# Kernel tuning notes

Hardware: AMD Instinct MI355X
Metric: run time of the kernel (lower is better)

The kernel has to match this reference:

```python
import jax, jax.numpy as jnp
import numpy as np

E = 128       # embed_dim
H = 128       # hidden_dim
NLABEL = 5
VOCAB = 50000
DEPTH = 18    # levels 0..17, complete binary tree
BRANCH = 2
N_NODES = 2 ** DEPTH - 1  # level-order layout: level l occupies [2^l-1, 2^(l+1)-1)


def setup_inputs() -> dict:
    key = jax.random.key(0)
    ks = jax.random.split(key, 24)

    def w(k, shape):
        return jax.random.normal(k, shape, dtype=jnp.float32) * 0.05

    inp = {
        "embeds": w(ks[0], (VOCAB, E)),
        "node_words": jax.random.randint(ks[1], (N_NODES,), 0, VOCAB),
        "node_labels": jax.random.randint(ks[2], (N_NODES,), 0, NLABEL),
        "depth": DEPTH,
        "branching": BRANCH,
    }
    # 8 gate linears: *x maps E->H, *h maps H->H (torch nn.Linear: y = x @ W.T + b)
    for j, nm in enumerate(["ix", "ih", "fx", "fh", "ox", "oh", "ux", "uh"]):
        in_dim = E if nm.endswith("x") else H
        inp["W" + nm] = w(ks[3 + 2 * j], (H, in_dim))
        inp["b" + nm] = w(ks[4 + 2 * j], (H,))
    inp["Wout"] = w(ks[20], (NLABEL, H))
    inp["bout"] = w(ks[21], (NLABEL,))
    return inp


def _lin(x, W, b):
    return x @ W.T + b


def _tree_lstm(embeds, node_words, node_labels, depth, branching,
               Wix, bix, Wih, bih, Wfx, bfx, Wfh, bfh,
               Wox, box, Woh, boh, Wux, bux, Wuh, buh, Wout, bout):
    b = branching
    hid = Wix.shape[0]
    loss = jnp.zeros((), dtype=embeds.dtype)
    child_c = child_h = None
    logp = None
    # bottom-up over levels (leaves first); level l has b^l nodes at offset (b^l-1)/(b-1)
    for l in range(depth - 1, -1, -1):
        n = b ** l
        off = (b ** l - 1) // (b - 1)
        x = embeds[node_words[off:off + n]]            # [n, E]
        if child_h is None:                            # leaves: zero child states
            h_sum = jnp.zeros((n, hid), dtype=embeds.dtype)
            c_agg = jnp.zeros((n, hid), dtype=embeds.dtype)
        else:
            ch = child_h.reshape(n, b, hid)            # children of each level-l node
            cc = child_c.reshape(n, b, hid)
            h_sum = ch.sum(axis=1)                     # child-sum
            f = jax.nn.sigmoid(_lin(x, Wfx, bfx)[:, None, :] + _lin(ch, Wfh, bfh))
            c_agg = (f * cc).sum(axis=1)               # sum_k f_k * c_k
        i = jax.nn.sigmoid(_lin(x, Wix, bix) + _lin(h_sum, Wih, bih))
        o = jax.nn.sigmoid(_lin(x, Wox, box) + _lin(h_sum, Woh, boh))
        u = jnp.tanh(_lin(x, Wux, bux) + _lin(h_sum, Wuh, buh))
        c = i * u + c_agg
        h = o * jnp.tanh(c)
        logp = jax.nn.log_softmax(_lin(h, Wout, bout), axis=-1)   # [n, NLABEL]
        lab = node_labels[off:off + n]
        loss = loss - logp[jnp.arange(n), lab].sum()              # NLL summed over nodes
        child_c, child_h = c, h
    return logp, loss  # logp from level 0 = root log-probs [1, NLABEL]


def reference(embeds, node_words, node_labels, depth, branching,
              Wix, bix, Wih, bih, Wfx, bfx, Wfh, bfh,
              Wox, box, Woh, boh, Wux, bux, Wuh, buh, Wout, bout):
    return _tree_lstm(embeds, node_words, node_labels, depth, branching,
                      Wix, bix, Wih, bih, Wfx, bfx, Wfh, bfh,
                      Wox, box, Woh, boh, Wux, bux, Wuh, buh, Wout, bout)
```

## Files before the change

kernel.cpp:

```cpp
#include <hip/hip_runtime.h>
#include <math.h>

#define DEPTH 18
#define NINT ((1 << (DEPTH - 1)) - 1)
#define LEAF_OFF ((1 << (DEPTH - 2)) - 1)
#define NVOCAB 50000
#define SAW 520
#define KTS 9
#define NEMB (NVOCAB * 128 / 4 / 256)

typedef unsigned short bf16raw;
typedef __bf16 bf16x8 __attribute__((ext_vector_type(8)));
typedef float f32x4 __attribute__((ext_vector_type(4)));
typedef short short8 __attribute__((ext_vector_type(8)));

__device__ __forceinline__ float sigm(float x) { return 1.0f / (1.0f + __expf(-x)); }
__device__ __forceinline__ float fast_tanh(float x) {
    float t = __expf(2.0f * x);
    return 1.0f - 2.0f / (t + 1.0f);
}

__device__ __forceinline__ float bf2f(bf16raw u) {
    union { unsigned int i; float f; } v;
    v.i = ((unsigned int)u) << 16;
    return v.f;
}
__device__ __forceinline__ bf16raw f2bf(float f) {
    union { float f; unsigned int i; } v;
    v.f = f;
    unsigned int r = v.i + 0x7FFFu + ((v.i >> 16) & 1u);
    return (bf16raw)(r >> 16);
}

#define SB() __builtin_amdgcn_sched_barrier(0)

__global__ __launch_bounds__(256) void k_prep_all(
    const float* __restrict__ embeds,
    const float* __restrict__ Wix, const float* __restrict__ bix,
    const float* __restrict__ Wih, const float* __restrict__ bih,
    const float* __restrict__ Wfx, const float* __restrict__ bfx,
    const float* __restrict__ Wfh, const float* __restrict__ bfh,
    const float* __restrict__ Wox, const float* __restrict__ box_,
    const float* __restrict__ Woh, const float* __restrict__ boh,
    const float* __restrict__ Wux, const float* __restrict__ bux,
    const float* __restrict__ Wuh, const float* __restrict__ buh,
    const float* __restrict__ Wout,
    bf16raw* __restrict__ embeds_bf,
    bf16raw* __restrict__ Bfrag, bf16raw* __restrict__ WoutFrag,
    float* __restrict__ bias_cat, float* __restrict__ partials)
{
    const int bid = blockIdx.x;
    const int t = threadIdx.x;
    if (bid < NEMB) {
        const int i = bid * 256 + t;
        float4 v = ((const float4*)embeds)[i];
        ushort4 o;
        o.x = f2bf(v.x); o.y = f2bf(v.y); o.z = f2bf(v.z); o.w = f2bf(v.w);
        ((ushort4*)embeds_bf)[i] = o;
        return;
    }
    if (bid == NEMB + 528) {
#pragma unroll
        for (int s = 0; s < 4; ++s) partials[t + 256 * s] = 0.f;
        return;
    }
    const int j = bid - NEMB;
    if (j >= 512) {
        const int col = j - 512;
        for (int k = t; k < 128; k += 256) {
            float v = (col < 5) ? Wout[col * 128 + k] : 0.f;
            WoutFrag[((k >> 5) * 64 + ((k >> 3) & 3) * 16 + col) * 8 + (k & 7)] = f2bf(v);
        }
        return;
    }
    const int gate = j >> 7, jj = j & 127;
    const float *Wx, *Wh, *bx, *bh;
    switch (gate) {
        case 0: Wx = Wix; Wh = Wih; bx = bix;  bh = bih; break;
        case 1: Wx = Wux; Wh = Wuh; bx = bux;  bh = buh; break;
        case 2: Wx = Wox; Wh = Woh; bx = box_; bh = boh; break;
        default: Wx = Wfx; Wh = Wfh; bx = bfx; bh = bfh; break;
    }
    const int coltile = (j >> 4) & 7, lr = j & 15;
    for (int k = t; k < 256; k += 256) {
        float v = (k < 128) ? Wx[jj * 128 + k] : Wh[jj * 128 + (k - 128)];
        const int idx = (((gate * 8 + coltile) * KTS + (k >> 5)) * 64
                         + ((k >> 3) & 3) * 16 + lr) * 8 + (k & 7);
        Bfrag[idx] = f2bf(v);
    }
    if (t == 0) bias_cat[j] = bx[jj] + bh[jj];
}

template<int CB>
__device__ __forceinline__ void lp_burst(const bf16raw* __restrict__ bfbase, int wcol,
                                         bf16x8 (&bb)[16])
{
#pragma unroll
    for (int kt = 0; kt < 4; ++kt)
#pragma unroll
        for (int j = 0; j < 4; ++j)
            bb[kt * 4 + j] = *(const bf16x8*)(bfbase +
                    (long)(((CB * 8 + (wcol >> 4) + j) * KTS + kt) * 512));
}

__device__ __forceinline__ void lp_mfma_all(const bf16raw* __restrict__ sA, int wrow,
                                            int lrow, int lquad,
                                            bf16x8 (&bb)[16], f32x4 (&acc)[2][4])
{
#pragma unroll
    for (int kt = 0; kt < 4; ++kt) {
        bf16x8 af[2];
#pragma unroll
        for (int i = 0; i < 2; ++i)
            af[i] = *(const bf16x8*)&sA[(wrow + i * 16 + lrow) * 136 + kt * 32 + lquad * 8];
#pragma unroll
        for (int i = 0; i < 2; ++i)
#pragma unroll
            for (int j = 0; j < 4; ++j)
                acc[i][j] = __builtin_amdgcn_mfma_f32_16x16x32_bf16(af[i], bb[kt * 4 + j], acc[i][j], 0, 0, 0);
    }
}

template<int CB>
__device__ __forceinline__ void lp_rungemm(const bf16raw* __restrict__ sA,
                                           const bf16raw* __restrict__ bfbase,
                                           int wrow, int wcol, int lrow, int lquad,
                                           f32x4 (&acc)[2][4])
{
#pragma unroll
    for (int i = 0; i < 2; i++)
#pragma unroll
        for (int j = 0; j < 4; j++) acc[i][j] = (f32x4){0.f, 0.f, 0.f, 0.f};
    bf16x8 bb[16];
    lp_burst<CB>(bfbase, wcol, bb);
    SB();
    lp_mfma_all(sA, wrow, lrow, lquad, bb, acc);
}

template<int G, int H>
__device__ __forceinline__ void load8(const bf16raw* __restrict__ bfbase, int w,
                                      bf16x8 (&bb)[8])
{
#pragma unroll
    for (int kt2 = 0; kt2 < 4; ++kt2)
#pragma unroll
        for (int jj = 0; jj < 2; ++jj)
            bb[kt2 * 2 + jj] = *(const bf16x8*)(bfbase +
                    (long)(((G * 8 + w * 2 + jj) * KTS + H * 4 + kt2) * 512));
}

template<int AB>
__device__ __forceinline__ void mfma4k(const bf16raw* __restrict__ sA, int lrow, int lquad,
                                       bf16x8 (&bb)[8], f32x4 (&acc)[2][2])
{
#pragma unroll
    for (int kt2 = 0; kt2 < 4; ++kt2) {
        bf16x8 af[2];
#pragma unroll
        for (int i = 0; i < 2; ++i)
            af[i] = *(const bf16x8*)&sA[(i * 16 + lrow) * SAW + (AB + kt2) * 32 + lquad * 8];
#pragma unroll
        for (int jj = 0; jj < 2; ++jj)
#pragma unroll
            for (int i = 0; i < 2; ++i)
                acc[i][jj] = __builtin_amdgcn_mfma_f32_16x16x32_bf16(af[i], bb[kt2 * 2 + jj], acc[i][jj], 0, 0, 0);
    }
}

__global__ __launch_bounds__(256, 3) void k_leafpre(
    const bf16raw* __restrict__ embeds_bf,
    const bf16raw* __restrict__ Bfrag, const float* __restrict__ bias_cat,
    const bf16raw* __restrict__ WoutFrag, const float* __restrict__ bout,
    bf16raw* __restrict__ hc_leaf, float* __restrict__ lossv6, int nvtot)
{
    const int vbase = blockIdx.x * 64;
    int nv = nvtot - vbase;
    if (nv > 64) nv = 64;
    if (nv <= 0) return;

    __shared__ __align__(16) bf16raw sA[64 * 136];
    __shared__ __align__(16) bf16raw sT[64 * 136];
    __shared__ float sLg[64 * 5];

    const int t = threadIdx.x;

    {
        const int row = t >> 2;
        const int co = (t & 3) * 32;
        const int arow = (row < nv) ? row : 0;
        const bf16raw* ax = embeds_bf + (long)(vbase + arow) * 128;
        *(short8*)&sA[row * 136 + co]      = *(const short8*)(ax + co);
        *(short8*)&sA[row * 136 + co + 8]  = *(const short8*)(ax + co + 8);
        *(short8*)&sA[row * 136 + co + 16] = *(const short8*)(ax + co + 16);
        *(short8*)&sA[row * 136 + co + 24] = *(const short8*)(ax + co + 24);
    }

    const int lane = t & 63;
    const int w = t >> 6;
    const int wrow = (w & 1) * 32;
    const int wcol = (w >> 1) * 64;
    const int lrow = lane & 15;
    const int lquad = lane >> 4;

    __syncthreads();

    const bf16raw* bfbase = Bfrag + (long)lane * 8;

    float tval[2][4][4];
    f32x4 acc[2][4];

    lp_rungemm<0>(sA, bfbase, wrow, wcol, lrow, lquad, acc);
#pragma unroll
    for (int i = 0; i < 2; i++)
#pragma unroll
        for (int jj = 0; jj < 4; jj++) {
            const float b = bias_cat[wcol + jj * 16 + lrow];
#pragma unroll
            for (int r = 0; r < 4; r++) tval[i][jj][r] = sigm(acc[i][jj][r] + b);
        }
    lp_rungemm<1>(sA, bfbase, wrow, wcol, lrow, lquad, acc);
#pragma unroll
    for (int i = 0; i < 2; i++)
#pragma unroll
        for (int jj = 0; jj < 4; jj++) {
            const float b = bias_cat[128 + wcol + jj * 16 + lrow];
#pragma unroll
            for (int r = 0; r < 4; r++) tval[i][jj][r] *= fast_tanh(acc[i][jj][r] + b);
        }
#pragma unroll
    for (int i = 0; i < 2; i++)
#pragma unroll
        for (int jj = 0; jj < 4; jj++)
#pragma unroll
            for (int r = 0; r < 4; r++) {
                const int m = wrow + i * 16 + lquad * 4 + r;
                const int j = wcol + jj * 16 + lrow;
                sT[m * 136 + j] = f2bf(tval[i][jj][r]);
            }
#pragma unroll
    for (int i = 0; i < 2; i++)
#pragma unroll
        for (int jj = 0; jj < 4; jj++)
#pragma unroll
            for (int r = 0; r < 4; r++) tval[i][jj][r] = fast_tanh(tval[i][jj][r]);
    __syncthreads();
#pragma unroll
    for (int s = 0; s < 4; ++s) {
        int ci = t + 256 * s;
        int row = ci >> 4, c8 = (ci & 15) * 8;
        if (row < nv)
            *(short8*)(hc_leaf + (long)(vbase + row) * 256 + 128 + c8) = *(const short8*)&sT[row * 136 + c8];
    }
    lp_rungemm<2>(sA, bfbase, wrow, wcol, lrow, lquad, acc);
    __syncthreads();
#pragma unroll
    for (int i = 0; i < 2; i++)
#pragma unroll
        for (int jj = 0; jj < 4; jj++) {
            const float b = bias_cat[256 + wcol + jj * 16 + lrow];
#pragma unroll
            for (int r = 0; r < 4; r++) {
                const int m = wrow + i * 16 + lquad * 4 + r;
                const int j = wcol + jj * 16 + lrow;
                sT[m * 136 + j] = f2bf(sigm(acc[i][jj][r] + b) * tval[i][jj][r]);
            }
        }
    __syncthreads();
#pragma unroll
    for (int s = 0; s < 4; ++s) {
        int ci = t + 256 * s;
        int row = ci >> 4, c8 = (ci & 15) * 8;
        if (row < nv)
            *(short8*)(hc_leaf + (long)(vbase + row) * 256 + c8) = *(const short8*)&sT[row * 136 + c8];
    }
    {
        f32x4 lacc = (f32x4){0.f, 0.f, 0.f, 0.f};
#pragma unroll
        for (int kt = 0; kt < 4; ++kt) {
            bf16x8 bfr = *(const bf16x8*)(WoutFrag + (long)((kt * 64 + lane) * 8));
            bf16x8 af = *(const bf16x8*)&sT[(w * 16 + lrow) * 136 + kt * 32 + lquad * 8];
            lacc = __builtin_amdgcn_mfma_f32_16x16x32_bf16(af, bfr, lacc, 0, 0, 0);
        }
        if (lrow < 5) {
            const float bl = bout[lrow];
#pragma unroll
            for (int r = 0; r < 4; ++r)
                sLg[(w * 16 + lquad * 4 + r) * 5 + lrow] = lacc[r] + bl;
        }
    }
    __syncthreads();
    if (t < 64 && t < nv) {
        float lg[5], mx = -1e30f;
#pragma unroll
        for (int l = 0; l < 5; l++) {
            lg[l] = sLg[t * 5 + l];
            mx = fmaxf(mx, lg[l]);
        }
        float se = 0.f;
#pragma unroll
        for (int l = 0; l < 5; l++) se += __expf(lg[l] - mx);
        float lse = __logf(se) + mx;
        float* dst = lossv6 + (long)(vbase + t) * 6;
#pragma unroll
        for (int l = 0; l < 5; l++) dst[l] = lg[l];
        dst[5] = lse;
    }
}

__global__ __launch_bounds__(256, 3) void k_level32(
    const bf16raw* __restrict__ embeds_bf, const int* __restrict__ words,
    const int* __restrict__ labels,
    bf16raw* __restrict__ h_all, bf16raw* __restrict__ c_all,
    const bf16raw* __restrict__ hc_leaf, const float* __restrict__ lossv6,
    const bf16raw* __restrict__ Bfrag, const bf16raw* __restrict__ WoutFrag,
    const float* __restrict__ bias_cat, const float* __restrict__ bout,
    float* __restrict__ partials, float* __restrict__ out,
    int off, int nm, int leafkids, int isroot)
{
    __shared__ __align__(16) bf16raw sA[32 * SAW];
    __shared__ __align__(16) bf16raw sCT[64 * 136];
    __shared__ float sLg[168];

    const int t = threadIdx.x;
    const int m0 = blockIdx.x * 32;

    {
        const int row = t >> 3;
        const int co = (t & 7) * 8;
        int mm = m0 + row; if (mm >= nm) mm = nm - 1;
        const long g = (long)off + mm;
        const bf16raw* px = embeds_bf + (long)words[g] * 128;
        const bf16raw *p1, *p2;
        if (leafkids) {
            p1 = hc_leaf + (long)words[2 * g + 1] * 256;
            p2 = hc_leaf + (long)words[2 * g + 2] * 256;
        } else {
            p1 = h_all + (2 * g + 1) * 128;
            p2 = h_all + (2 * g + 2) * 128;
        }
        short8 vx0 = *(const short8*)(px + co);
        short8 vx1 = *(const short8*)(px + 64 + co);
        short8 h10 = *(const short8*)(p1 + co);
        short8 h11 = *(const short8*)(p1 + 64 + co);
        short8 h20 = *(const short8*)(p2 + co);
        short8 h21 = *(const short8*)(p2 + 64 + co);
        short8 hs0, hs1;
#pragma unroll
        for (int e = 0; e < 8; ++e) {
            hs0[e] = (short)f2bf(bf2f((bf16raw)(unsigned short)h10[e]) +
                                 bf2f((bf16raw)(unsigned short)h20[e]));
            hs1[e] = (short)f2bf(bf2f((bf16raw)(unsigned short)h11[e]) +
                                 bf2f((bf16raw)(unsigned short)h21[e]));
        }
        *(short8*)&sA[row * SAW + co]        = vx0;
        *(short8*)&sA[row * SAW + 64 + co]   = vx1;
        *(short8*)&sA[row * SAW + 128 + co]  = hs0;
        *(short8*)&sA[row * SAW + 192 + co]  = hs1;
        *(short8*)&sA[row * SAW + 256 + co]  = h10;
        *(short8*)&sA[row * SAW + 320 + co]  = h11;
        *(short8*)&sA[row * SAW + 384 + co]  = h20;
        *(short8*)&sA[row * SAW + 448 + co]  = h21;
    }
    {
        const int slot = t >> 2;
        const int cc8 = (t & 3) * 8;
        int mm = m0 + (slot >> 1); if (mm >= nm) mm = nm - 1;
        const long g = (long)off + mm;
        const long cg = 2 * g + 1 + (slot & 1);
        const bf16raw* pc = leafkids ? (hc_leaf + (long)words[cg] * 256 + 128)
                                     : (c_all + cg * 128);
#pragma unroll
        for (int s = 0; s < 4; ++s)
            *(short8*)&sCT[slot * 136 + s * 32 + cc8] = *(const short8*)(pc + s * 32 + cc8);
    }

    const int lane = t & 63;
    const int w = t >> 6;
    const int lrow = lane & 15;
    const int lquad = lane >> 4;

    float bias[4][2];
#pragma unroll
    for (int g = 0; g < 4; ++g)
#pragma unroll
        for (int jj = 0; jj < 2; ++jj)
            bias[g][jj] = bias_cat[g * 128 + w * 32 + jj * 16 + lrow];

    __syncthreads();

    const bf16raw* bfbase = Bfrag + (long)lane * 8;

    f32x4 acc[2][2];
    f32x4 fx[2][2];
    float si[2][2][4];
    float cc[2][2][4];
    float hh[2][2][4];
    bf16x8 bbA[8], bbB[8];

#define ZACC() { _Pragma("unroll") for (int i_ = 0; i_ < 2; ++i_) \
                 _Pragma("unroll") for (int j_ = 0; j_ < 2; ++j_) \
                     acc[i_][j_] = (f32x4){0.f, 0.f, 0.f, 0.f}; }

    load8<0, 0>(bfbase, w, bbA);
    load8<0, 1>(bfbase, w, bbB);
    SB();
    ZACC();
    mfma4k<0>(sA, lrow, lquad, bbA, acc); SB();
    load8<1, 0>(bfbase, w, bbA); SB();
    mfma4k<4>(sA, lrow, lquad, bbB, acc); SB();
    load8<1, 1>(bfbase, w, bbB); SB();
#pragma unroll
    for (int i = 0; i < 2; ++i)
#pragma unroll
        for (int jj = 0; jj < 2; ++jj)
#pragma unroll
            for (int r = 0; r < 4; ++r)
                si[i][jj][r] = sigm(acc[i][jj][r] + bias[0][jj]);
    ZACC();
    mfma4k<0>(sA, lrow, lquad, bbA, acc); SB();
    load8<3, 0>(bfbase, w, bbA); SB();
    mfma4k<4>(sA, lrow, lquad, bbB, acc); SB();
    load8<3, 1>(bfbase, w, bbB); SB();
#pragma unroll
    for (int i = 0; i < 2; ++i)
#pragma unroll
        for (int jj = 0; jj < 2; ++jj)
#pragma unroll
            for (int r = 0; r < 4; ++r)
                cc[i][jj][r] = si[i][jj][r] * fast_tanh(acc[i][jj][r] + bias[1][jj]);
    ZACC();
    mfma4k<0>(sA, lrow, lquad, bbA, acc);
    SB();
#pragma unroll
    for (int i = 0; i < 2; ++i)
#pragma unroll
        for (int jj = 0; jj < 2; ++jj) fx[i][jj] = acc[i][jj];
    mfma4k<8>(sA, lrow, lquad, bbB, acc);
    SB();
    load8<2, 0>(bfbase, w, bbA);
    SB();
#pragma unroll
    for (int i = 0; i < 2; ++i)
#pragma unroll
        for (int jj = 0; jj < 2; ++jj) {
            const int j = w * 32 + jj * 16 + lrow;
#pragma unroll
            for (int r = 0; r < 4; ++r) {
                const int m = i * 16 + lquad * 4 + r;
                cc[i][jj][r] += sigm(acc[i][jj][r] + bias[3][jj]) * bf2f(sCT[(2 * m) * 136 + j]);
            }
        }
#pragma unroll
    for (int i = 0; i < 2; ++i)
#pragma unroll
        for (int jj = 0; jj < 2; ++jj) acc[i][jj] = fx[i][jj];
    mfma4k<12>(sA, lrow, lquad, bbB, acc);
    SB();
    load8<2, 1>(bfbase, w, bbB);
    SB();
#pragma unroll
    for (int i = 0; i < 2; ++i)
#pragma unroll
        for (int jj = 0; jj < 2; ++jj) {
            const int j = w * 32 + jj * 16 + lrow;
#pragma unroll
            for (int r = 0; r < 4; ++r) {
                const int m = i * 16 + lquad * 4 + r;
                cc[i][jj][r] += sigm(acc[i][jj][r] + bias[3][jj]) * bf2f(sCT[(2 * m + 1) * 136 + j]);
            }
        }
    ZACC();
    mfma4k<0>(sA, lrow, lquad, bbA, acc);
    mfma4k<4>(sA, lrow, lquad, bbB, acc);
    SB();
#pragma unroll
    for (int i = 0; i < 2; ++i)
#pragma unroll
        for (int jj = 0; jj < 2; ++jj)
#pragma unroll
            for (int r = 0; r < 4; ++r)
                hh[i][jj][r] = sigm(acc[i][jj][r] + bias[2][jj]) * fast_tanh(cc[i][jj][r]);
#undef ZACC

    __syncthreads();

#pragma unroll
    for (int i = 0; i < 2; ++i)
#pragma unroll
        for (int jj = 0; jj < 2; ++jj) {
            const int j = w * 32 + jj * 16 + lrow;
#pragma unroll
            for (int r = 0; r < 4; ++r) {
                const int m = i * 16 + lquad * 4 + r;
                sCT[m * 136 + j] = f2bf(cc[i][jj][r]);
                sCT[(32 + m) * 136 + j] = f2bf(hh[i][jj][r]);
            }
        }
    __syncthreads();

#pragma unroll
    for (int q = 0; q < 4; ++q) {
        int ci = t + 256 * q;
        int row = ci >> 4;
        int c8 = (ci & 15) * 8;
        int m = row & 31;
        if (m0 + m < nm) {
            bf16raw* dst = (row < 32) ? c_all : h_all;
            *(short8*)(dst + ((long)off + m0 + m) * 128 + c8) = *(const short8*)&sCT[row * 136 + c8];
        }
    }

    if (w == 0) {
        f32x4 lacc[2];
        lacc[0] = (f32x4){0.f, 0.f, 0.f, 0.f};
        lacc[1] = (f32x4){0.f, 0.f, 0.f, 0.f};
#pragma unroll
        for (int kt = 0; kt < 4; ++kt) {
            bf16x8 bfr = *(const bf16x8*)(WoutFrag + (long)((kt * 64 + lane) * 8));
#pragma unroll
            for (int i = 0; i < 2; ++i) {
                bf16x8 af = *(const bf16x8*)&sCT[(32 + i * 16 + lrow) * 136 + kt * 32 + lquad * 8];
                lacc[i] = __builtin_amdgcn_mfma_f32_16x16x32_bf16(af, bfr, lacc[i], 0, 0, 0);
            }
        }
        if (lrow < 5) {
            const float bl = bout[lrow];
#pragma unroll
            for (int i = 0; i < 2; ++i)
#pragma unroll
                for (int r = 0; r < 4; ++r)
                    sLg[(i * 16 + lquad * 4 + r) * 5 + lrow] = lacc[i][r] + bl;
        }
    }
    __syncthreads();

    if (t < 32 && m0 + t < nm) {
        const long g = (long)off + m0 + t;
        float lgv[5], mx = -1e30f;
#pragma unroll
        for (int l = 0; l < 5; ++l) {
            lgv[l] = sLg[t * 5 + l];
            mx = fmaxf(mx, lgv[l]);
        }
        float se = 0.f;
#pragma unroll
        for (int l = 0; l < 5; ++l) se += __expf(lgv[l] - mx);
        float lse = __logf(se) + mx;
        float lossNode = lse - lgv[labels[g]];
        if (leafkids) {
            const float* lv1 = lossv6 + (long)words[2 * g + 1] * 6;
            const float* lv2 = lossv6 + (long)words[2 * g + 2] * 6;
            lossNode += (lv1[5] - lv1[labels[2 * g + 1]])
                      + (lv2[5] - lv2[labels[2 * g + 2]]);
        }
        if (isroot) {
            sLg[164] = lossNode;
#pragma unroll
            for (int l = 0; l < 5; ++l) out[l] = lgv[l] - lse;
        } else {
            atomicAdd(&partials[(int)(g & 1023)], lossNode);
        }
    }

    if (isroot) {
        __syncthreads();
        float s = 0.f;
        for (int i2 = t; i2 < 1024; i2 += 256) s += partials[i2];
#pragma unroll
        for (int d = 32; d > 0; d >>= 1) s += __shfl_down(s, d);
        if ((t & 63) == 0) sLg[160 + (t >> 6)] = s;
        __syncthreads();
        if (t == 0)
            out[5] = sLg[160] + sLg[161] + sLg[162] + sLg[163] + sLg[164];
    }
}

extern "C" void kernel_launch(void* const* d_in, const int* in_sizes, int n_in,
                              void* d_out, int out_size, void* d_ws, size_t ws_size,
                              hipStream_t stream)
{
    const float* embeds = (const float*)d_in[0];
    const int* words = (const int*)d_in[1];
    const int* labels = (const int*)d_in[2];
    const float* Wix = (const float*)d_in[5],  *bix  = (const float*)d_in[6];
    const float* Wih = (const float*)d_in[7],  *bih  = (const float*)d_in[8];
    const float* Wfx = (const float*)d_in[9],  *bfx  = (const float*)d_in[10];
    const float* Wfh = (const float*)d_in[11], *bfh  = (const float*)d_in[12];
    const float* Wox = (const float*)d_in[13], *box_ = (const float*)d_in[14];
    const float* Woh = (const float*)d_in[15], *boh  = (const float*)d_in[16];
    const float* Wux = (const float*)d_in[17], *bux  = (const float*)d_in[18];
    const float* Wuh = (const float*)d_in[19], *buh  = (const float*)d_in[20];
    const float* Wout = (const float*)d_in[21], *bout = (const float*)d_in[22];
    float* out = (float*)d_out;

    char* ws = (char*)d_ws;
    const size_t treeElems = (size_t)NINT * 128;
    bf16raw* h_all = (bf16raw*)ws;
    bf16raw* c_all = h_all + treeElems;
    bf16raw* embeds_bf = c_all + treeElems;
    bf16raw* Bfrag = embeds_bf + (size_t)NVOCAB * 128;
    bf16raw* WoutFrag = Bfrag + 4 * 8 * KTS * 512;
    bf16raw* hc_leaf = WoutFrag + 4 * 64 * 8;
    float* lossv6 = (float*)(hc_leaf + (size_t)NVOCAB * 256);
    float* bias_cat = lossv6 + (size_t)NVOCAB * 6;
    float* partials = bias_cat + 512;

    k_prep_all<<<NEMB + 528 + 1, 256, 0, stream>>>(
        embeds, Wix, bix, Wih, bih, Wfx, bfx, Wfh, bfh,
        Wox, box_, Woh, boh, Wux, bux, Wuh, buh, Wout,
        embeds_bf, Bfrag, WoutFrag, bias_cat, partials);

    k_leafpre<<<(NVOCAB + 63) / 64, 256, 0, stream>>>(
        embeds_bf, Bfrag, bias_cat, WoutFrag, bout, hc_leaf, lossv6, NVOCAB);

    for (int l = DEPTH - 2; l >= 0; --l) {
        const int n = 1 << l;
        k_level32<<<dim3((n + 31) / 32), 256, 0, stream>>>(
            embeds_bf, words, labels, h_all, c_all, hc_leaf, lossv6,
            Bfrag, WoutFrag, bias_cat, bout, partials, out,
            n - 1, n, (l == DEPTH - 2) ? 1 : 0, (l == 0) ? 1 : 0);
    }
}
```

Before: 366.5 us.

## Fuse two tree levels per launch with in-block parent computation

```diff
diff --git a/kernel.cpp b/kernel.cpp
--- a/kernel.cpp
+++ b/kernel.cpp
@@ -3,7 +3,6 @@
 
 #define DEPTH 18
 #define NINT ((1 << (DEPTH - 1)) - 1)
-#define LEAF_OFF ((1 << (DEPTH - 2)) - 1)
 #define NVOCAB 50000
 #define SAW 520
 #define KTS 9
@@ -167,6 +166,19 @@
     }
 }
 
+template<int AB>
+__device__ __forceinline__ void mfma4k1(const bf16raw* __restrict__ sA, int lrow, int lquad,
+                                        bf16x8 (&bb)[8], f32x4 (&acc)[2])
+{
+#pragma unroll
+    for (int kt2 = 0; kt2 < 4; ++kt2) {
+        bf16x8 af = *(const bf16x8*)&sA[lrow * SAW + (AB + kt2) * 32 + lquad * 8];
+#pragma unroll
+        for (int jj = 0; jj < 2; ++jj)
+            acc[jj] = __builtin_amdgcn_mfma_f32_16x16x32_bf16(af, bb[kt2 * 2 + jj], acc[jj], 0, 0, 0);
+    }
+}
+
 __global__ __launch_bounds__(256, 3) void k_leafpre(
     const bf16raw* __restrict__ embeds_bf,
     const bf16raw* __restrict__ Bfrag, const float* __restrict__ bias_cat,
@@ -304,6 +316,402 @@
 #pragma unroll
         for (int l = 0; l < 5; l++) dst[l] = lg[l];
         dst[5] = lse;
+    }
+}
+
+__global__ __launch_bounds__(256, 3) void k_pair(
+    const bf16raw* __restrict__ embeds_bf, const int* __restrict__ words,
+    const int* __restrict__ labels,
+    bf16raw* __restrict__ h_all, bf16raw* __restrict__ c_all,
+    const bf16raw* __restrict__ hc_leaf, const float* __restrict__ lossv6,
+    const bf16raw* __restrict__ Bfrag, const bf16raw* __restrict__ WoutFrag,
+    const float* __restrict__ bias_cat, const float* __restrict__ bout,
+    float* __restrict__ partials,
+    int offP, int nP, int leafkids)
+{
+    __shared__ __align__(16) bf16raw sA[32 * SAW];
+    __shared__ __align__(16) bf16raw sCT[64 * 136];
+    __shared__ float sLg[160];
+
+    const int t = threadIdx.x;
+    const int offC = 2 * offP + 1;
+    const int nmC = 2 * nP;
+    const int m0C = blockIdx.x * 32;
+    const int m0P = blockIdx.x * 16;
+
+    const int lane = t & 63;
+    const int w = t >> 6;
+    const int lrow = lane & 15;
+    const int lquad = lane >> 4;
+    const bf16raw* bfbase = Bfrag + (long)lane * 8;
+
+    float bias[4][2];
+#pragma unroll
+    for (int g = 0; g < 4; ++g)
+#pragma unroll
+        for (int jj = 0; jj < 2; ++jj)
+            bias[g][jj] = bias_cat[g * 128 + w * 32 + jj * 16 + lrow];
+
+    {
+        const int row = t >> 3;
+        const int co = (t & 7) * 8;
+        int mm = m0C + row; if (mm >= nmC) mm = nmC - 1;
+        const long g = (long)offC + mm;
+        const bf16raw* px = embeds_bf + (long)words[g] * 128;
+        const bf16raw *p1, *p2;
+        if (leafkids) {
+            p1 = hc_leaf + (long)words[2 * g + 1] * 256;
+            p2 = hc_leaf + (long)words[2 * g + 2] * 256;
+        } else {
+            p1 = h_all + (2 * g + 1) * 128;
+            p2 = h_all + (2 * g + 2) * 128;
+        }
+        short8 vx0 = *(const short8*)(px + co);
+        short8 vx1 = *(const short8*)(px + 64 + co);
+        short8 h10 = *(const short8*)(p1 + co);
+        short8 h11 = *(const short8*)(p1 + 64 + co);
+        short8 h20 = *(const short8*)(p2 + co);
+        short8 h21 = *(const short8*)(p2 + 64 + co);
+        short8 hs0, hs1;
+#pragma unroll
+        for (int e = 0; e < 8; ++e) {
+            hs0[e] = (short)f2bf(bf2f((bf16raw)(unsigned short)h10[e]) +
+                                 bf2f((bf16raw)(unsigned short)h20[e]));
+            hs1[e] = (short)f2bf(bf2f((bf16raw)(unsigned short)h11[e]) +
+                                 bf2f((bf16raw)(unsigned short)h21[e]));
+        }
+        *(short8*)&sA[row * SAW + co]        = vx0;
+        *(short8*)&sA[row * SAW + 64 + co]   = vx1;
+        *(short8*)&sA[row * SAW + 128 + co]  = hs0;
+        *(short8*)&sA[row * SAW + 192 + co]  = hs1;
+        *(short8*)&sA[row * SAW + 256 + co]  = h10;
+        *(short8*)&sA[row * SAW + 320 + co]  = h11;
+        *(short8*)&sA[row * SAW + 384 + co]  = h20;
+        *(short8*)&sA[row * SAW + 448 + co]  = h21;
+    }
+    {
+        const int slot = t >> 2;
+        const int cc8 = (t & 3) * 8;
+        int mm = m0C + (slot >> 1); if (mm >= nmC) mm = nmC - 1;
+        const long g = (long)offC + mm;
+        const long cg = 2 * g + 1 + (slot & 1);
+        const bf16raw* pc = leafkids ? (hc_leaf + (long)words[cg] * 256 + 128)
+                                     : (c_all + cg * 128);
+#pragma unroll
+        for (int s = 0; s < 4; ++s)
+            *(short8*)&sCT[slot * 136 + s * 32 + cc8] = *(const short8*)(pc + s * 32 + cc8);
+    }
+    __syncthreads();
+
+    {
+        f32x4 acc[2][2];
+        f32x4 fx[2][2];
+        float si[2][2][4];
+        float cc[2][2][4];
+        float hh[2][2][4];
+        bf16x8 bbA[8], bbB[8];
+
+#define ZACC() { _Pragma("unroll") for (int i_ = 0; i_ < 2; ++i_) \
+                 _Pragma("unroll") for (int j_ = 0; j_ < 2; ++j_) \
+                     acc[i_][j_] = (f32x4){0.f, 0.f, 0.f, 0.f}; }
+
+        load8<0, 0>(bfbase, w, bbA);
+        load8<0, 1>(bfbase, w, bbB);
+        SB();
+        ZACC();
+        mfma4k<0>(sA, lrow, lquad, bbA, acc); SB();
+        load8<1, 0>(bfbase, w, bbA); SB();
+        mfma4k<4>(sA, lrow, lquad, bbB, acc); SB();
+        load8<1, 1>(bfbase, w, bbB); SB();
+#pragma unroll
+        for (int i = 0; i < 2; ++i)
+#pragma unroll
+            for (int jj = 0; jj < 2; ++jj)
+#pragma unroll
+                for (int r = 0; r < 4; ++r)
+                    si[i][jj][r] = sigm(acc[i][jj][r] + bias[0][jj]);
+        ZACC();
+        mfma4k<0>(sA, lrow, lquad, bbA, acc); SB();
+        load8<3, 0>(bfbase, w, bbA); SB();
+        mfma4k<4>(sA, lrow, lquad, bbB, acc); SB();
+        load8<3, 1>(bfbase, w, bbB); SB();
+#pragma unroll
+        for (int i = 0; i < 2; ++i)
+#pragma unroll
+            for (int jj = 0; jj < 2; ++jj)
+#pragma unroll
+                for (int r = 0; r < 4; ++r)
+                    cc[i][jj][r] = si[i][jj][r] * fast_tanh(acc[i][jj][r] + bias[1][jj]);
+        ZACC();
+        mfma4k<0>(sA, lrow, lquad, bbA, acc);
+        SB();
+#pragma unroll
+        for (int i = 0; i < 2; ++i)
+#pragma unroll
+            for (int jj = 0; jj < 2; ++jj) fx[i][jj] = acc[i][jj];
+        mfma4k<8>(sA, lrow, lquad, bbB, acc);
+        SB();
+        load8<2, 0>(bfbase, w, bbA);
+        SB();
+#pragma unroll
+        for (int i = 0; i < 2; ++i)
+#pragma unroll
+            for (int jj = 0; jj < 2; ++jj) {
+                const int j = w * 32 + jj * 16 + lrow;
+#pragma unroll
+                for (int r = 0; r < 4; ++r) {
+                    const int m = i * 16 + lquad * 4 + r;
+                    cc[i][jj][r] += sigm(acc[i][jj][r] + bias[3][jj]) * bf2f(sCT[(2 * m) * 136 + j]);
+                }
+            }
+#pragma unroll
+        for (int i = 0; i < 2; ++i)
+#pragma unroll
+            for (int jj = 0; jj < 2; ++jj) acc[i][jj] = fx[i][jj];
+        mfma4k<12>(sA, lrow, lquad, bbB, acc);
+        SB();
+        load8<2, 1>(bfbase, w, bbB);
+        SB();
+#pragma unroll
+        for (int i = 0; i < 2; ++i)
+#pragma unroll
+            for (int jj = 0; jj < 2; ++jj) {
+                const int j = w * 32 + jj * 16 + lrow;
+#pragma unroll
+                for (int r = 0; r < 4; ++r) {
+                    const int m = i * 16 + lquad * 4 + r;
+                    cc[i][jj][r] += sigm(acc[i][jj][r] + bias[3][jj]) * bf2f(sCT[(2 * m + 1) * 136 + j]);
+                }
+            }
+        ZACC();
+        mfma4k<0>(sA, lrow, lquad, bbA, acc);
+        mfma4k<4>(sA, lrow, lquad, bbB, acc);
+        SB();
+#pragma unroll
+        for (int i = 0; i < 2; ++i)
+#pragma unroll
+            for (int jj = 0; jj < 2; ++jj)
+#pragma unroll
+                for (int r = 0; r < 4; ++r)
+                    hh[i][jj][r] = sigm(acc[i][jj][r] + bias[2][jj]) * fast_tanh(cc[i][jj][r]);
+#undef ZACC
+
+        __syncthreads();
+
+#pragma unroll
+        for (int i = 0; i < 2; ++i)
+#pragma unroll
+            for (int jj = 0; jj < 2; ++jj) {
+                const int j = w * 32 + jj * 16 + lrow;
+#pragma unroll
+                for (int r = 0; r < 4; ++r) {
+                    const int m = i * 16 + lquad * 4 + r;
+                    sCT[m * 136 + j] = f2bf(cc[i][jj][r]);
+                    sCT[(32 + m) * 136 + j] = f2bf(hh[i][jj][r]);
+                }
+            }
+    }
+    __syncthreads();
+
+    if (w == 0) {
+        f32x4 lacc[2];
+        lacc[0] = (f32x4){0.f, 0.f, 0.f, 0.f};
+        lacc[1] = (f32x4){0.f, 0.f, 0.f, 0.f};
+#pragma unroll
+        for (int kt = 0; kt < 4; ++kt) {
+            bf16x8 bfr = *(const bf16x8*)(WoutFrag + (long)((kt * 64 + lane) * 8));
+#pragma unroll
+            for (int i = 0; i < 2; ++i) {
+                bf16x8 af = *(const bf16x8*)&sCT[(32 + i * 16 + lrow) * 136 + kt * 32 + lquad * 8];
+                lacc[i] = __builtin_amdgcn_mfma_f32_16x16x32_bf16(af, bfr, lacc[i], 0, 0, 0);
+            }
+        }
+        if (lrow < 5) {
+            const float bl = bout[lrow];
+#pragma unroll
+            for (int i = 0; i < 2; ++i)
+#pragma unroll
+                for (int r = 0; r < 4; ++r)
+                    sLg[(i * 16 + lquad * 4 + r) * 5 + lrow] = lacc[i][r] + bl;
+        }
+    }
+    __syncthreads();
+
+    if (t < 32 && m0C + t < nmC) {
+        const long g = (long)offC + m0C + t;
+        float lgv[5], mx = -1e30f;
+#pragma unroll
+        for (int l = 0; l < 5; ++l) {
+            lgv[l] = sLg[t * 5 + l];
+            mx = fmaxf(mx, lgv[l]);
+        }
+        float se = 0.f;
+#pragma unroll
+        for (int l = 0; l < 5; ++l) se += __expf(lgv[l] - mx);
+        float lse = __logf(se) + mx;
+        float lossNode = lse - lgv[labels[g]];
+        if (leafkids) {
+            const float* lv1 = lossv6 + (long)words[2 * g + 1] * 6;
+            const float* lv2 = lossv6 + (long)words[2 * g + 2] * 6;
+            lossNode += (lv1[5] - lv1[labels[2 * g + 1]])
+                      + (lv2[5] - lv2[labels[2 * g + 2]]);
+        }
+        atomicAdd(&partials[(int)(g & 1023)], lossNode);
+    }
+    {
+        const int rowP = t >> 4;
+        const int co = (t & 15) * 8;
+        int pp = m0P + rowP; if (pp >= nP) pp = nP - 1;
+        const long gP = (long)offP + pp;
+        const int dp = pp - m0P;
+        const bf16raw* px = embeds_bf + (long)words[gP] * 128;
+        short8 vx = *(const short8*)(px + co);
+        short8 h1 = *(short8*)&sCT[(32 + 2 * dp) * 136 + co];
+        short8 h2 = *(short8*)&sCT[(32 + 2 * dp + 1) * 136 + co];
+        short8 hs;
+#pragma unroll
+        for (int e = 0; e < 8; ++e)
+            hs[e] = (short)f2bf(bf2f((bf16raw)(unsigned short)h1[e]) +
+                                bf2f((bf16raw)(unsigned short)h2[e]));
+        *(short8*)&sA[rowP * SAW + co]       = vx;
+        *(short8*)&sA[rowP * SAW + 128 + co] = hs;
+        *(short8*)&sA[rowP * SAW + 256 + co] = h1;
+        *(short8*)&sA[rowP * SAW + 384 + co] = h2;
+    }
+    __syncthreads();
+
+    {
+        f32x4 acc[2];
+        f32x4 fx[2];
+        float si[2][4];
+        float cc[2][4];
+        float hh[2][4];
+        bf16x8 bbA[8], bbB[8];
+
+#define PZ() { acc[0] = (f32x4){0.f,0.f,0.f,0.f}; acc[1] = (f32x4){0.f,0.f,0.f,0.f}; }
+
+        load8<0, 0>(bfbase, w, bbA);
+        load8<0, 1>(bfbase, w, bbB);
+        SB();
+        PZ();
+        mfma4k1<0>(sA, lrow, lquad, bbA, acc); SB();
+        load8<1, 0>(bfbase, w, bbA); SB();
+        mfma4k1<4>(sA, lrow, lquad, bbB, acc); SB();
+        load8<1, 1>(bfbase, w, bbB); SB();
+#pragma unroll
+        for (int jj = 0; jj < 2; ++jj)
+#pragma unroll
+            for (int r = 0; r < 4; ++r)
+                si[jj][r] = sigm(acc[jj][r] + bias[0][jj]);
+        PZ();
+        mfma4k1<0>(sA, lrow, lquad, bbA, acc); SB();
+        load8<3, 0>(bfbase, w, bbA); SB();
+        mfma4k1<4>(sA, lrow, lquad, bbB, acc); SB();
+        load8<3, 1>(bfbase, w, bbB); SB();
+#pragma unroll
+        for (int jj = 0; jj < 2; ++jj)
+#pragma unroll
+            for (int r = 0; r < 4; ++r)
+                cc[jj][r] = si[jj][r] * fast_tanh(acc[jj][r] + bias[1][jj]);
+        PZ();
+        mfma4k1<0>(sA, lrow, lquad, bbA, acc);
+        SB();
+        fx[0] = acc[0]; fx[1] = acc[1];
+        mfma4k1<8>(sA, lrow, lquad, bbB, acc);
+        SB();
+        load8<2, 0>(bfbase, w, bbA);
+        SB();
+#pragma unroll
+        for (int jj = 0; jj < 2; ++jj) {
+            const int j = w * 32 + jj * 16 + lrow;
+#pragma unroll
+            for (int r = 0; r < 4; ++r) {
+                const int m = lquad * 4 + r;
+                cc[jj][r] += sigm(acc[jj][r] + bias[3][jj]) * bf2f(sCT[(2 * m) * 136 + j]);
+            }
+        }
+        acc[0] = fx[0]; acc[1] = fx[1];
+        mfma4k1<12>(sA, lrow, lquad, bbB, acc);
+        SB();
+        load8<2, 1>(bfbase, w, bbB);
+        SB();
+#pragma unroll
+        for (int jj = 0; jj < 2; ++jj) {
+            const int j = w * 32 + jj * 16 + lrow;
+#pragma unroll
+            for (int r = 0; r < 4; ++r) {
+                const int m = lquad * 4 + r;
+                cc[jj][r] += sigm(acc[jj][r] + bias[3][jj]) * bf2f(sCT[(2 * m + 1) * 136 + j]);
+            }
+        }
+        PZ();
+        mfma4k1<0>(sA, lrow, lquad, bbA, acc);
+        mfma4k1<4>(sA, lrow, lquad, bbB, acc);
+        SB();
+#pragma unroll
+        for (int jj = 0; jj < 2; ++jj)
+#pragma unroll
+            for (int r = 0; r < 4; ++r)
+                hh[jj][r] = sigm(acc[jj][r] + bias[2][jj]) * fast_tanh(cc[jj][r]);
+#undef PZ
+
+        __syncthreads();
+
+#pragma unroll
+        for (int jj = 0; jj < 2; ++jj) {
+            const int j = w * 32 + jj * 16 + lrow;
+#pragma unroll
+            for (int r = 0; r < 4; ++r) {
+                const int m = lquad * 4 + r;
+                sCT[m * 136 + j] = f2bf(cc[jj][r]);
+                sCT[(16 + m) * 136 + j] = f2bf(hh[jj][r]);
+            }
+        }
+    }
+    __syncthreads();
+
+#pragma unroll
+    for (int q = 0; q < 2; ++q) {
+        int ci = t + 256 * q;
+        int row = ci >> 4;
+        int c8 = (ci & 15) * 8;
+        int m = row & 15;
+        if (m0P + m < nP) {
+            bf16raw* dst = (row < 16) ? c_all : h_all;
+            *(short8*)(dst + ((long)offP + m0P + m) * 128 + c8) = *(const short8*)&sCT[row * 136 + c8];
+        }
+    }
+
+    if (w == 0) {
+        f32x4 lacc = (f32x4){0.f, 0.f, 0.f, 0.f};
+#pragma unroll
+        for (int kt = 0; kt < 4; ++kt) {
+            bf16x8 bfr = *(const bf16x8*)(WoutFrag + (long)((kt * 64 + lane) * 8));
+            bf16x8 af = *(const bf16x8*)&sCT[(16 + lrow) * 136 + kt * 32 + lquad * 8];
+            lacc = __builtin_amdgcn_mfma_f32_16x16x32_bf16(af, bfr, lacc, 0, 0, 0);
+        }
+        if (lrow < 5) {
+            const float bl = bout[lrow];
+#pragma unroll
+            for (int r = 0; r < 4; ++r)
+                sLg[(lquad * 4 + r) * 5 + lrow] = lacc[r] + bl;
+        }
+    }
+    __syncthreads();
+
+    if (t < 16 && m0P + t < nP) {
+        const long g = (long)offP + m0P + t;
+        float lgv[5], mx = -1e30f;
+#pragma unroll
+        for (int l = 0; l < 5; ++l) {
+            lgv[l] = sLg[t * 5 + l];
+            mx = fmaxf(mx, lgv[l]);
+        }
+        float se = 0.f;
+#pragma unroll
+        for (int l = 0; l < 5; ++l) se += __expf(lgv[l] - mx);
+        float lse = __logf(se) + mx;
+        atomicAdd(&partials[(int)(g & 1023)], lse - lgv[labels[g]]);
     }
 }
 
@@ -613,11 +1021,15 @@
     k_leafpre<<<(NVOCAB + 63) / 64, 256, 0, stream>>>(
         embeds_bf, Bfrag, bias_cat, WoutFrag, bout, hc_leaf, lossv6, NVOCAB);
 
-    for (int l = DEPTH - 2; l >= 0; --l) {
-        const int n = 1 << l;
-        k_level32<<<dim3((n + 31) / 32), 256, 0, stream>>>(
+    for (int l = DEPTH - 3; l >= 1; l -= 2) {
+        const int nP = 1 << l;
+        k_pair<<<dim3((nP + 15) / 16), 256, 0, stream>>>(
             embeds_bf, words, labels, h_all, c_all, hc_leaf, lossv6,
-            Bfrag, WoutFrag, bias_cat, bout, partials, out,
-            n - 1, n, (l == DEPTH - 2) ? 1 : 0, (l == 0) ? 1 : 0);
-    }
-}
+            Bfrag, WoutFrag, bias_cat, bout, partials,
+            nP - 1, nP, (l == DEPTH - 3) ? 1 : 0);
+    }
+    k_level32<<<dim3(1), 256, 0, stream>>>(
+        embeds_bf, words, labels, h_all, c_all, hc_leaf, lossv6,
+        Bfrag, WoutFrag, bias_cat, bout, partials, out,
+        0, 1, 0, 1);
+}
```

Result: slower. 379.6 us (+3.6%).
